# Optimization experiments

Measured on AMD Instinct MI355X. Metric: run time of the kernel, lower is better.

## Reference

```python
import jax, jax.numpy as jnp
import numpy as np
jax.config.update("jax_enable_x64", True)

TAPS, DELAY = 5, 3
EPS = 1e-6        # DNN_WPE.eps: power clamp before WPE
WPE_EPS = 1e-10   # wpe_one_iteration eps: inverse-power clamp + diag loading


def _signal_framing(Y, L):
    # Y: (..., T) -> (..., T-L+1, L) sliding frames (as_strided equivalent)
    T = Y.shape[-1]
    idx = jnp.arange(T - L + 1)[:, None] + jnp.arange(L)[None, :]
    return Y[..., idx]


def _wpe_one_iteration(Y, power, taps, delay):
    # Y: (B,F,C,T) complex128, power: (B,F,T) float64
    B, F, C, T = Y.shape
    inv_power = 1.0 / jnp.maximum(power, WPE_EPS)
    Tp = T - delay - taps + 1
    # tap-stacked delayed signal, taps axis reversed: (B,F,C,Tp,taps)
    Psi = _signal_framing(Y, taps)[..., :Tp, :][..., ::-1]
    Psi_n = Psi.conj() * inv_power[:, :, None, delay + taps - 1:, None]
    # covariance R: (B,F,taps*C,taps*C); cross-corr P: (B,F,taps,C_e,C_d)
    R = jnp.einsum("bfdtk,bfetl->bfkdle", Psi_n, Psi).reshape(B, F, taps * C, taps * C)
    P = jnp.einsum("bfdtk,bfet->bfked", Psi_n, Y[..., delay + taps - 1:])
    # v: (B,F,C_e,taps*C_d); conj filter G = inv(R) @ v^T  (X = v @ inv(R)^T)
    v = P.transpose(0, 1, 3, 2, 4).reshape(B, F, C, taps * C)
    eye = jnp.eye(taps * C, dtype=R.dtype)
    tr = jnp.trace(R, axis1=-2, axis2=-1).real[..., None, None] / (taps * C)
    G = jnp.linalg.solve(R + WPE_EPS * tr * eye, v.transpose(0, 1, 3, 2))
    G = G.reshape(B, F, taps, C, C)  # (B,F,tau,d,e) conjugated filter matrix
    # reverb tail: sum over taps of filtered, delayed signal
    tail = jnp.zeros_like(Y)
    for tau in range(taps):  # taps=5, small fixed loop
        s = delay + tau
        contrib = jnp.einsum("bfde,bfdt->bfet", G[:, :, tau], Y[..., : T - s])
        tail = tail.at[..., s:].add(contrib)
    return Y - tail


def setup_inputs() -> dict:
    key = jax.random.key(0)
    k1, k2, k3 = jax.random.split(key, 3)
    B, T, C, F = 4, 512, 8, 257
    data_real = jax.random.normal(k1, (B, T, C, F), dtype=jnp.float32)
    data_imag = jax.random.normal(k2, (B, T, C, F), dtype=jnp.float32)
    ilens = jax.random.randint(k3, (B,), 256, T + 1)
    return {"data_real": data_real, "data_imag": data_imag, "ilens": ilens}


def reference(data_real, data_imag, ilens):
    # (B,T,C,F) -> (B,F,C,T)
    data = (data_real + 1j * data_imag).transpose(0, 3, 2, 1)
    # power averaged over channels, clamped (B,F,T)
    power = jnp.maximum(jnp.mean(data.real ** 2 + data.imag ** 2, axis=-2), EPS)
    enh = _wpe_one_iteration(data.astype(jnp.complex128), power.astype(jnp.float64), TAPS, DELAY)
    enh = enh.astype(jnp.complex64)
    T = enh.shape[-1]
    pad = (jnp.arange(T)[None, :] >= ilens[:, None])[:, None, None, :]  # (B,1,1,T)
    enh = jnp.where(pad, 0.0 + 0.0j, enh)
    enh = enh.transpose(0, 3, 2, 1)  # back to (B,T,C,F)
    return enh.real, enh.imag, power
```

## Files before the change

### kernel.cpp

```cpp
#include <hip/hip_runtime.h>
#include <hip/hip_fp16.h>

#define B_ 4
#define T_ 512
#define C_ 8
#define F_ 257
#define TAPS 5
#define DELAY 3
#define N_ 40
#define NA 48
#define TP 505
#define T0 7
#define BF (B_*F_)
#define BTCF ((size_t)B_*T_*C_*F_)
#define YSH 532
#define YPAD 8
#define AUGSZ 1180
#define ZSD 36

typedef _Float16 half8 __attribute__((ext_vector_type(8)));
typedef float floatx4 __attribute__((ext_vector_type(4)));
typedef uint32_t uint32x4 __attribute__((ext_vector_type(4)));

__device__ inline uint32_t h2mul(uint32_t a, uint32_t b) {
    __half2 r = __hmul2(__builtin_bit_cast(__half2, a), __builtin_bit_cast(__half2, b));
    return __builtin_bit_cast(uint32_t, r);
}
__device__ inline uint32_t packf16(float2 v) {
    __half2 h = __floats2half2_rn(v.x, v.y);
    return __builtin_bit_cast(uint32_t, h);
}
__device__ inline half8 mkfrag(uint32_t a, uint32_t b, uint32_t c, uint32_t d) {
    uint32x4 v = {a, b, c, d};
    return __builtin_bit_cast(half8, v);
}
__device__ inline int rowoff(int i) {
    return i * 49 - ((i * (i - 1)) >> 1);
}

struct Frag { half8 X; half8 Y; };

__device__ inline Frag build2(const uint32_t* p, uint32_t sw0, uint32_t sw1,
                              uint32_t sw2, uint32_t sw3) {
    uint32_t q0 = p[0], q1 = p[1], q2 = p[2], q3 = p[3];
    uint32_t q4 = p[4], q5 = p[5], q6 = p[6], q7 = p[7];
    uint32_t x0 = __builtin_amdgcn_perm(q1, q0, 0x05040100);
    uint32_t y0 = __builtin_amdgcn_perm(q1, q0, 0x07060302);
    uint32_t x1 = __builtin_amdgcn_perm(q3, q2, 0x05040100);
    uint32_t y1 = __builtin_amdgcn_perm(q3, q2, 0x07060302);
    uint32_t x2 = __builtin_amdgcn_perm(q5, q4, 0x05040100);
    uint32_t y2 = __builtin_amdgcn_perm(q5, q4, 0x07060302);
    uint32_t x3 = __builtin_amdgcn_perm(q7, q6, 0x05040100);
    uint32_t y3 = __builtin_amdgcn_perm(q7, q6, 0x07060302);
    Frag f;
    f.X = mkfrag(h2mul(x0, sw0), h2mul(x1, sw1), h2mul(x2, sw2), h2mul(x3, sw3));
    f.Y = mkfrag(h2mul(y0, sw0), h2mul(y1, sw1), h2mul(y2, sw2), h2mul(y3, sw3));
    return f;
}
__device__ inline int zs_off(int j) {
    return (j < N_) ? (j & 7) * YSH + (YPAD + 4 - (j >> 3)) : (j - N_) * YSH + (YPAD + T0);
}

__global__ __launch_bounds__(256) void k_fused(const float* __restrict__ in_re,
                                               const float* __restrict__ in_im,
                                               const int* __restrict__ ilens,
                                               float* __restrict__ out_re,
                                               float* __restrict__ out_im,
                                               float* __restrict__ pow_out) {
    __shared__ uint32_t sYh[C_ * YSH];
    __shared__ __align__(16) float uScr[640];
    __shared__ __align__(16) uint32_t sw_pk[256];
    __shared__ __align__(16) float2 sAugU[AUGSZ];
    float* sPow = uScr;
    float2* sGT = (float2*)uScr;
    int tid = threadIdx.x;

    int bid = blockIdx.x;
    int xcd = bid & 7, slot = bid >> 3;
    int w = (xcd < 4) ? xcd * 129 + slot : 516 + (xcd - 4) * 128 + slot;
    int b = w / F_;
    int f = w - b * F_;
    int ilen = ilens[b];
    const float* pre = in_re + (size_t)b * T_ * C_ * F_ + f;
    const float* pim = in_im + (size_t)b * T_ * C_ * F_ + f;

    {
        int t0 = tid, t1 = tid + 256;
        float s0 = 0.f, s1 = 0.f;
#pragma unroll 2
        for (int c = 0; c < C_; ++c) {
            size_t a0 = ((size_t)t0 * C_ + c) * F_;
            size_t a1 = ((size_t)t1 * C_ + c) * F_;
            float xr0 = pre[a0], xi0 = pim[a0];
            float xr1 = pre[a1], xi1 = pim[a1];
            sYh[c * YSH + YPAD + t0] = packf16(make_float2(xr0, xi0));
            sYh[c * YSH + YPAD + t1] = packf16(make_float2(xr1, xi1));
            s0 += xr0 * xr0 + xi0 * xi0;
            s1 += xr1 * xr1 + xi1 * xi1;
        }
        if (tid < 20) {
            int z = (tid < 8) ? tid : (512 + tid);
#pragma unroll
            for (int c = 0; c < C_; ++c) sYh[c * YSH + z] = 0;
        }
        s0 = fmaxf(s0 * (1.0f / C_), 1e-6f);
        s1 = fmaxf(s1 * (1.0f / C_), 1e-6f);
        pow_out[(size_t)w * T_ + t0] = s0;
        pow_out[(size_t)w * T_ + t1] = s1;
        sPow[t0] = s0;
        sPow[t1] = s1;
    }
    __syncthreads();

    {
        int k0 = 2 * tid, k1 = k0 + 1;
        float w0 = (k0 < TP) ? rsqrtf(sPow[k0 + T0]) : 0.f;
        float w1 = (k1 < TP) ? rsqrtf(sPow[k1 + T0]) : 0.f;
        sw_pk[tid] = packf16(make_float2(w0, w1));
    }
    __syncthreads();

    int wv = tid >> 6, ln = tid & 63;
    int kg = ln >> 4;
    if (wv < 3) {
        int r16 = ln & 15;
        int offB = zs_off(wv * 16 + r16);
#pragma unroll 1
        for (int mt = 0; mt < 3; ++mt) {
            int offA = zs_off(mt * 16 + r16);
            floatx4 aRe = {0.f, 0.f, 0.f, 0.f};
            floatx4 aIm = {0.f, 0.f, 0.f, 0.f};
#pragma unroll 2
            for (int ks = 0; ks < 16; ++ks) {
                int kbase = ks * 32 + kg * 8;
                uint32x4 sv = *(const uint32x4*)&sw_pk[kbase >> 1];
                Frag B = build2(&sYh[offB + kbase], sv[0], sv[1], sv[2], sv[3]);
                Frag A = build2(&sYh[offA + kbase], sv[0], sv[1], sv[2], sv[3]);
                half8 nYa = -A.Y;
                aRe = __builtin_amdgcn_mfma_f32_16x16x32_f16(A.X, B.X, aRe, 0, 0, 0);
                aRe = __builtin_amdgcn_mfma_f32_16x16x32_f16(A.Y, B.Y, aRe, 0, 0, 0);
                aIm = __builtin_amdgcn_mfma_f32_16x16x32_f16(A.X, B.Y, aIm, 0, 0, 0);
                aIm = __builtin_amdgcn_mfma_f32_16x16x32_f16(nYa, B.X, aIm, 0, 0, 0);
            }
#pragma unroll
            for (int r = 0; r < 4; ++r) {
                int m = mt * 16 + kg * 4 + r;
                int col = wv * 16 + r16;
                if (m < N_ && col >= m)
                    sAugU[rowoff(m) + col - m] = make_float2(aRe[r], aIm[r]);
            }
        }
    }
    __syncthreads();

    if (tid < 64) {
        float dv = (tid < N_) ? sAugU[rowoff(tid)].x : 0.f;
#pragma unroll
        for (int off = 32; off; off >>= 1) dv += __shfl_xor(dv, off, 64);
        if (tid < N_) sAugU[rowoff(tid)].x += 1e-10f * dv / N_;
    }
    __syncthreads();

    {
        int ri = tid >> 4, ci = tid & 15;
#pragma unroll 1
        for (int p = 0; p < N_ - 1; ++p) {
            int rop = rowoff(p);
            float2 piv = sAugU[rop];
            float dnm = piv.x * piv.x + piv.y * piv.y;
            float pix = piv.x / dnm, piy = -piv.y / dnm;
#pragma unroll 1
            for (int i = p + 1 + ri; i < N_; i += 16) {
                float2 api = sAugU[rop + i - p];
                float mx = api.x * pix + api.y * piy;
                float my = api.x * piy - api.y * pix;
                int roi = rowoff(i) - i;
#pragma unroll 1
                for (int j = i + ci; j < NA; j += 16) {
                    float2 apj = sAugU[rop + j - p];
                    float2 v = sAugU[roi + j];
                    v.x -= mx * apj.x - my * apj.y;
                    v.y -= mx * apj.y + my * apj.x;
                    sAugU[roi + j] = v;
                }
            }
            __syncthreads();
        }
    }
    {
        int bc = tid & 7, br = tid >> 3;
#pragma unroll 1
        for (int p = N_ - 1; p > 0; --p) {
            int rop = rowoff(p);
            float2 piv = sAugU[rop];
            float dnm = piv.x * piv.x + piv.y * piv.y;
            float pix = piv.x / dnm, piy = -piv.y / dnm;
            float2 rhs = sAugU[rop + N_ + bc - p];
            float xr = rhs.x * pix - rhs.y * piy;
            float xi = rhs.x * piy + rhs.y * pix;
#pragma unroll 1
            for (int i = br; i < p; i += 32) {
                int roi = rowoff(i) - i;
                float2 aip = sAugU[roi + p];
                float2 v = sAugU[roi + N_ + bc];
                v.x -= aip.x * xr - aip.y * xi;
                v.y -= aip.x * xi + aip.y * xr;
                sAugU[roi + N_ + bc] = v;
            }
            __syncthreads();
        }
    }
    for (int idx = tid; idx < N_ * C_; idx += 256) {
        int j = idx >> 3;
        int e = idx & 7;
        int roj = rowoff(j);
        float2 piv = sAugU[roj];
        float dnm = piv.x * piv.x + piv.y * piv.y;
        float pix = piv.x / dnm, piy = -piv.y / dnm;
        float2 rhs = sAugU[roj + N_ + e - j];
        int tau = j >> 3, d = j & 7;
        sGT[(e * C_ + d) * TAPS + tau] =
            make_float2(rhs.x * pix - rhs.y * piy, rhs.x * piy + rhs.y * pix);
    }
    __syncthreads();

    uint32_t* zRe = (uint32_t*)sAugU;
    uint32_t* zIm = zRe + 32 * ZSD;
    half8 aFr[2], aFi[2];
    {
        int m = ln & 15;
#pragma unroll
        for (int ks = 0; ks < 2; ++ks) {
            half8 hr = {}, hi = {};
#pragma unroll
            for (int q = 0; q < 8; ++q) {
                int j = ks * 32 + kg * 8 + q;
                float gx = 0.f, gy = 0.f;
                if (m < 8 && j < N_) {
                    float2 g = sGT[(m * C_ + (j & 7)) * TAPS + (j >> 3)];
                    gx = g.x; gy = g.y;
                }
                hr[q] = (_Float16)gx;
                hi[q] = (_Float16)gy;
            }
            aFr[ks] = hr;
            aFi[ks] = hi;
        }
    }
    for (int idx = tid; idx < 2 * 32 * ZSD; idx += 256) zRe[idx] = 0;
    __syncthreads();

#pragma unroll 1
    for (int ch = 0; ch < 16; ++ch) {
        int c0 = ch * 32;
        for (int idx = tid; idx < 640; idx += 256) {
            int jp = idx >> 5, tl = idx & 31;
            int j0 = 2 * jp, j1 = j0 + 1;
            int base = c0 + tl + (YPAD - 3);
            uint32_t y0 = sYh[(j0 & 7) * YSH + base - (j0 >> 3)];
            uint32_t y1 = sYh[(j1 & 7) * YSH + base - (j1 >> 3)];
            zRe[tl * ZSD + jp] = __builtin_amdgcn_perm(y1, y0, 0x05040100);
            zIm[tl * ZSD + jp] = __builtin_amdgcn_perm(y1, y0, 0x07060302);
        }
        __syncthreads();
        if (wv < 2) {
            floatx4 accR = {0.f, 0.f, 0.f, 0.f};
            floatx4 accI = {0.f, 0.f, 0.f, 0.f};
            int trow = wv * 16 + (ln & 15);
#pragma unroll
            for (int ks = 0; ks < 2; ++ks) {
                int o = trow * ZSD + ks * 16 + kg * 4;
                half8 Br = __builtin_bit_cast(half8, *(const uint32x4*)&zRe[o]);
                half8 Bi = __builtin_bit_cast(half8, *(const uint32x4*)&zIm[o]);
                half8 nFi = -aFi[ks];
                accR = __builtin_amdgcn_mfma_f32_16x16x32_f16(aFr[ks], Br, accR, 0, 0, 0);
                accR = __builtin_amdgcn_mfma_f32_16x16x32_f16(nFi, Bi, accR, 0, 0, 0);
                accI = __builtin_amdgcn_mfma_f32_16x16x32_f16(aFr[ks], Bi, accI, 0, 0, 0);
                accI = __builtin_amdgcn_mfma_f32_16x16x32_f16(aFi[ks], Br, accI, 0, 0, 0);
            }
            if (kg < 2) {
                int tg = c0 + trow;
                bool dead = (tg >= ilen);
#pragma unroll
                for (int r = 0; r < 4; ++r) {
                    int e = kg * 4 + r;
                    size_t a = ((size_t)tg * C_ + e) * F_;
                    float ex = pre[a] - accR[r];
                    float ey = pim[a] - accI[r];
                    if (dead) { ex = 0.f; ey = 0.f; }
                    size_t o = (size_t)b * T_ * C_ * F_ + f + a;
                    out_re[o] = ex;
                    out_im[o] = ey;
                }
            }
        }
        __syncthreads();
    }
}

extern "C" void kernel_launch(void* const* d_in, const int* in_sizes, int n_in,
                              void* d_out, int out_size, void* d_ws, size_t ws_size,
                              hipStream_t stream) {
    const float* in_re = (const float*)d_in[0];
    const float* in_im = (const float*)d_in[1];
    const int* ilens = (const int*)d_in[2];

    float* out_re = (float*)d_out;
    float* out_im = out_re + BTCF;
    float* out_pw = out_im + BTCF;

    k_fused<<<BF, 256, 0, stream>>>(in_re, in_im, ilens, out_re, out_im, out_pw);
}
```

Measured before the change: 210.4 us.

## Use all four waves for tail MFMA and read residual from shared fp16 copy

The tail-filter stage now processes 64 time steps per chunk, so all four waves run MFMAs instead of two, which halves the number of chunk iterations. To fit in shared memory, the real and imaginary Z tiles are built one after the other in a single buffer, with extra barriers between them. The residual subtraction now reads the fp16-packed signal already held in shared memory instead of reloading the fp32 input from global memory. This removes a second global read but loses precision in the passthrough term. The channel loop unroll in the load phase is also raised.

```diff
diff --git a/kernel.cpp b/kernel.cpp
--- a/kernel.cpp
+++ b/kernel.cpp
@@ -30,6 +30,10 @@
     __half2 h = __floats2half2_rn(v.x, v.y);
     return __builtin_bit_cast(uint32_t, h);
 }
+__device__ inline float2 unpackf16(uint32_t u) {
+    __half2 h = __builtin_bit_cast(__half2, u);
+    return make_float2(__low2float(h), __high2float(h));
+}
 __device__ inline half8 mkfrag(uint32_t a, uint32_t b, uint32_t c, uint32_t d) {
     uint32x4 v = {a, b, c, d};
     return __builtin_bit_cast(half8, v);
@@ -87,7 +91,7 @@
     {
         int t0 = tid, t1 = tid + 256;
         float s0 = 0.f, s1 = 0.f;
-#pragma unroll 2
+#pragma unroll 4
         for (int c = 0; c < C_; ++c) {
             size_t a0 = ((size_t)t0 * C_ + c) * F_;
             size_t a1 = ((size_t)t1 * C_ + c) * F_;
@@ -224,8 +228,7 @@
     }
     __syncthreads();
 
-    uint32_t* zRe = (uint32_t*)sAugU;
-    uint32_t* zIm = zRe + 32 * ZSD;
+    uint32_t* zBuf = (uint32_t*)sAugU;
     half8 aFr[2], aFi[2];
     {
         int m = ln & 15;
@@ -247,51 +250,62 @@
             aFi[ks] = hi;
         }
     }
-    for (int idx = tid; idx < 2 * 32 * ZSD; idx += 256) zRe[idx] = 0;
-    __syncthreads();
-
-#pragma unroll 1
-    for (int ch = 0; ch < 16; ++ch) {
-        int c0 = ch * 32;
-        for (int idx = tid; idx < 640; idx += 256) {
-            int jp = idx >> 5, tl = idx & 31;
+    for (int idx = tid; idx < 64 * ZSD; idx += 256) zBuf[idx] = 0;
+    __syncthreads();
+
+    int trow = wv * 16 + (ln & 15);
+#pragma unroll 1
+    for (int ch = 0; ch < 8; ++ch) {
+        int c0 = ch * 64;
+        for (int idx = tid; idx < 1280; idx += 256) {
+            int jp = idx >> 6, tl = idx & 63;
             int j0 = 2 * jp, j1 = j0 + 1;
             int base = c0 + tl + (YPAD - 3);
             uint32_t y0 = sYh[(j0 & 7) * YSH + base - (j0 >> 3)];
             uint32_t y1 = sYh[(j1 & 7) * YSH + base - (j1 >> 3)];
-            zRe[tl * ZSD + jp] = __builtin_amdgcn_perm(y1, y0, 0x05040100);
-            zIm[tl * ZSD + jp] = __builtin_amdgcn_perm(y1, y0, 0x07060302);
+            zBuf[tl * ZSD + jp] = __builtin_amdgcn_perm(y1, y0, 0x05040100);
         }
         __syncthreads();
-        if (wv < 2) {
-            floatx4 accR = {0.f, 0.f, 0.f, 0.f};
-            floatx4 accI = {0.f, 0.f, 0.f, 0.f};
-            int trow = wv * 16 + (ln & 15);
-#pragma unroll
-            for (int ks = 0; ks < 2; ++ks) {
-                int o = trow * ZSD + ks * 16 + kg * 4;
-                half8 Br = __builtin_bit_cast(half8, *(const uint32x4*)&zRe[o]);
-                half8 Bi = __builtin_bit_cast(half8, *(const uint32x4*)&zIm[o]);
-                half8 nFi = -aFi[ks];
-                accR = __builtin_amdgcn_mfma_f32_16x16x32_f16(aFr[ks], Br, accR, 0, 0, 0);
-                accR = __builtin_amdgcn_mfma_f32_16x16x32_f16(nFi, Bi, accR, 0, 0, 0);
-                accI = __builtin_amdgcn_mfma_f32_16x16x32_f16(aFr[ks], Bi, accI, 0, 0, 0);
-                accI = __builtin_amdgcn_mfma_f32_16x16x32_f16(aFi[ks], Br, accI, 0, 0, 0);
-            }
-            if (kg < 2) {
-                int tg = c0 + trow;
-                bool dead = (tg >= ilen);
-#pragma unroll
-                for (int r = 0; r < 4; ++r) {
-                    int e = kg * 4 + r;
-                    size_t a = ((size_t)tg * C_ + e) * F_;
-                    float ex = pre[a] - accR[r];
-                    float ey = pim[a] - accI[r];
-                    if (dead) { ex = 0.f; ey = 0.f; }
-                    size_t o = (size_t)b * T_ * C_ * F_ + f + a;
-                    out_re[o] = ex;
-                    out_im[o] = ey;
-                }
+        floatx4 accR = {0.f, 0.f, 0.f, 0.f};
+        floatx4 accI = {0.f, 0.f, 0.f, 0.f};
+#pragma unroll
+        for (int ks = 0; ks < 2; ++ks) {
+            int o = trow * ZSD + ks * 16 + kg * 4;
+            half8 Br = __builtin_bit_cast(half8, *(const uint32x4*)&zBuf[o]);
+            accR = __builtin_amdgcn_mfma_f32_16x16x32_f16(aFr[ks], Br, accR, 0, 0, 0);
+            accI = __builtin_amdgcn_mfma_f32_16x16x32_f16(aFi[ks], Br, accI, 0, 0, 0);
+        }
+        __syncthreads();
+        for (int idx = tid; idx < 1280; idx += 256) {
+            int jp = idx >> 6, tl = idx & 63;
+            int j0 = 2 * jp, j1 = j0 + 1;
+            int base = c0 + tl + (YPAD - 3);
+            uint32_t y0 = sYh[(j0 & 7) * YSH + base - (j0 >> 3)];
+            uint32_t y1 = sYh[(j1 & 7) * YSH + base - (j1 >> 3)];
+            zBuf[tl * ZSD + jp] = __builtin_amdgcn_perm(y1, y0, 0x07060302);
+        }
+        __syncthreads();
+#pragma unroll
+        for (int ks = 0; ks < 2; ++ks) {
+            int o = trow * ZSD + ks * 16 + kg * 4;
+            half8 Bi = __builtin_bit_cast(half8, *(const uint32x4*)&zBuf[o]);
+            half8 nFi = -aFi[ks];
+            accR = __builtin_amdgcn_mfma_f32_16x16x32_f16(nFi, Bi, accR, 0, 0, 0);
+            accI = __builtin_amdgcn_mfma_f32_16x16x32_f16(aFr[ks], Bi, accI, 0, 0, 0);
+        }
+        if (kg < 2) {
+            int tg = c0 + trow;
+            bool dead = (tg >= ilen);
+#pragma unroll
+            for (int r = 0; r < 4; ++r) {
+                int e = kg * 4 + r;
+                float2 cf = unpackf16(sYh[e * YSH + YPAD + tg]);
+                float ex = cf.x - accR[r];
+                float ey = cf.y - accI[r];
+                if (dead) { ex = 0.f; ey = 0.f; }
+                size_t o = (size_t)b * T_ * C_ * F_ + ((size_t)tg * C_ + e) * F_ + f;
+                out_re[o] = ex;
+                out_im[o] = ey;
             }
         }
         __syncthreads();
```

Measured after the change: 189.4 us. 1.11x faster.
